# Performance work log

Measured on AMD Instinct MI355X. Metric: run time of the kernel, lower is better.

## Reference

```python
import jax, jax.numpy as jnp
import numpy as np

B, C, H, W = 4, 256, 64, 64
NHEAD = 8
KH = KW = 3          # partition = [3, 3] -> 9-token windows, stride 1, padding 1
EPS = 1e-5           # torch LayerNorm default


def setup_inputs() -> dict:
    key = jax.random.key(0)
    ks = jax.random.split(key, 3)
    s = 1.0 / np.sqrt(C)  # xavier-ish scale
    return {
        "src": jax.random.normal(ks[0], (B, C, H, W), jnp.float32),
        "ln_w": jnp.ones((C,), jnp.float32),
        "ln_b": jnp.zeros((C,), jnp.float32),
        "in_proj_w": jax.random.normal(ks[1], (3 * C, C), jnp.float32) * s,
        "in_proj_b": jnp.zeros((3 * C,), jnp.float32),
        "out_proj_w": jax.random.normal(ks[2], (C, C), jnp.float32) * s,
        "out_proj_b": jnp.zeros((C,), jnp.float32),
    }


def reference(src, ln_w, ln_b, in_proj_w, in_proj_b, out_proj_w, out_proj_b):
    b, c, h, w = src.shape
    L = h * w
    S = KH * KW  # 9 tokens per local window
    # --- Unfold: overlapping 3x3 windows, padding 1, stride 1 (torch.nn.Unfold order: c major, kernel pos minor)
    xp = jnp.pad(src, ((0, 0), (0, 0), (1, 1), (1, 1)))
    patches = jnp.stack(
        [xp[:, :, i : i + h, j : j + w] for i in range(KH) for j in range(KW)], axis=2
    )  # [b, c, 9, h, w]
    x = patches.reshape(b, c, S, L).transpose(2, 0, 3, 1).reshape(S, b * L, c)  # [S, bL, c]
    # --- Pre-norm (norm1); note: pos embed in the source is overwritten (q = k = src2), FFN is dead code
    mu = x.mean(-1, keepdims=True)
    var = ((x - mu) ** 2).mean(-1, keepdims=True)
    x2 = (x - mu) / jnp.sqrt(var + EPS) * ln_w + ln_b
    # --- MultiheadAttention (self-attn, eval mode -> no dropout)
    qkv = jnp.einsum("sbc,dc->sbd", x2, in_proj_w) + in_proj_b  # [S, bL, 3c]
    q, k, v = jnp.split(qkv, 3, axis=-1)
    dh = c // NHEAD
    scale = dh ** -0.5
    q = q.reshape(S, b * L, NHEAD, dh) * scale
    k = k.reshape(S, b * L, NHEAD, dh)
    v = v.reshape(S, b * L, NHEAD, dh)
    scores = jnp.einsum("sbhd,tbhd->bhst", q, k)        # [bL, H, 9, 9]
    attn = jax.nn.softmax(scores, axis=-1)
    o = jnp.einsum("bhst,tbhd->sbhd", attn, v).reshape(S, b * L, c)
    o = jnp.einsum("sbc,dc->sbd", o, out_proj_w) + out_proj_b
    y = x + o  # residual
    # --- Fold back (kernel 1x1, stride 1): each output pixel = its window's center token
    center = y[S // 2]  # [bL, c]
    return center.reshape(b, L, c).transpose(0, 2, 1).reshape(b, c, h, w)
```

## Files before the change

### kernel.cpp

```cpp
#include <hip/hip_runtime.h>
#include <math.h>


#define NPIX 16384
#define HW   4096
#define CDIM 256

typedef short  bf16x8 __attribute__((ext_vector_type(8)));
typedef float  f32x4  __attribute__((ext_vector_type(4)));
typedef unsigned short u16x8 __attribute__((ext_vector_type(8)));

__device__ inline float bf2f(unsigned short u) {
    unsigned v = ((unsigned)u) << 16;
    return __builtin_bit_cast(float, v);
}
__device__ inline unsigned short f2bf(float f) {
    unsigned u = __builtin_bit_cast(unsigned, f);
    u += 0x7FFFu + ((u >> 16) & 1u);
    return (unsigned short)(u >> 16);
}

__global__ __launch_bounds__(256) void k_prep(const float* __restrict__ Wqkv,
                                              const float* __restrict__ Wout,
                                              const float* __restrict__ bqkv,
                                              const float* __restrict__ lnb,
                                              unsigned short* __restrict__ Wqkvbf,
                                              unsigned short* __restrict__ Woutbf,
                                              float* __restrict__ pads) {
    int bid = blockIdx.x, t = threadIdx.x;
    if (bid < 768) {
        int i = bid * 256 + t;
        Wqkvbf[i] = f2bf(Wqkv[i]);
    } else if (bid < 1024) {
        int i = (bid - 768) * 256 + t;
        Woutbf[i] = f2bf(Wout[i]);
    } else {
        int d = (bid - 1024) * 256 + t;
        int row = 256 + d;
        const float* wrow = Wqkv + (size_t)row * CDIM;
        float s = bqkv[row];
        for (int c = 0; c < CDIM; ++c) s += lnb[c] * wrow[c];
        pads[d] = s;
    }
}

__device__ inline void stageW32(const unsigned short* __restrict__ g,
                                unsigned short* lds, int t) {
    int lane = t & 63;
    int wv   = t >> 6;
    int rin  = lane >> 2;
    int slot = lane & 3;
    #pragma unroll
    for (int it = 0; it < 4; ++it) {
        int rbase = (wv * 4 + it) * 16;
        int row = rbase + rin;
        const unsigned short* src = g + (size_t)row * 256 + ((slot ^ (row & 3)) * 8);
        __builtin_amdgcn_global_load_lds(
            (const __attribute__((address_space(1))) void*)src,
            (__attribute__((address_space(3))) void*)(lds + rbase * 32),
            16, 0, 0);
    }
}

__global__ __launch_bounds__(256) void k_ln_qkv(const float* __restrict__ src,
                                                const float* __restrict__ lnw,
                                                const float* __restrict__ lnb,
                                                const unsigned short* __restrict__ Wbf,
                                                const float* __restrict__ bias,
                                                unsigned short* __restrict__ qkvbf) {
    __shared__ unsigned short As[32 * 256];
    __shared__ unsigned short Bs[2][256 * 32];

    int t = threadIdx.x;
    int bid = blockIdx.x;
    int sb = (bid & 7) * 64 + (bid >> 3);
    int n0 = sb * 32;
    int b = n0 >> 12, p0 = n0 & 4095;

    stageW32(Wbf, Bs[0], t);

    float* red  = (float*)(&Bs[1][0]);
    float* red2 = red + 264;
    float* muv  = red + 528;
    float* rsv  = red + 560;
    int pix = t & 31, q = t >> 5;
    const float* sp = src + ((size_t)b * CDIM) * HW + p0 + pix;
    float x[32];
    float sum = 0.f, sq = 0.f;
    #pragma unroll
    for (int i = 0; i < 32; ++i) {
        x[i] = sp[(size_t)(q * 32 + i) * HW];
        sum += x[i]; sq += x[i] * x[i];
    }
    red[q * 33 + pix] = sum; red2[q * 33 + pix] = sq;
    __syncthreads();
    if (t < 32) {
        float s = 0.f, s2 = 0.f;
        #pragma unroll
        for (int qq = 0; qq < 8; ++qq) { s += red[qq * 33 + t]; s2 += red2[qq * 33 + t]; }
        float mu = s * (1.f / 256.f);
        float var = fmaxf(s2 * (1.f / 256.f) - mu * mu, 0.f);
        muv[t] = mu; rsv[t] = rsqrtf(var + 1e-5f);
    }
    __syncthreads();
    {
        float mu = muv[pix], rs = rsv[pix];
        #pragma unroll
        for (int c8 = 0; c8 < 4; ++c8) {
            u16x8 o8;
            #pragma unroll
            for (int j = 0; j < 8; ++j) {
                int c = q * 32 + c8 * 8 + j;
                float xn = (x[c8 * 8 + j] - mu) * rs * lnw[c] + lnb[c];
                o8[j] = f2bf(xn);
            }
            int chunk = q * 4 + c8;
            *(u16x8*)((char*)As + (pix * 512 + (((chunk & 7) ^ (pix & 7)) | (chunk & 24)) * 16)) = o8;
        }
    }
    __syncthreads();

    int lane = t & 63, wv = t >> 6;
    int lr = lane & 15, lg = lane >> 4;

    for (int pass = 0; pass < 3; ++pass) {
        f32x4 acc[2][4] = {};
        #pragma unroll
        for (int kc = 0; kc < 8; ++kc) {
            int s = pass * 8 + kc;
            if (s < 23) {
                int ns = s + 1;
                stageW32(Wbf + (size_t)((ns >> 3) * 256) * 256 + (ns & 7) * 32,
                         Bs[ns & 1], t);
            }
            const unsigned short* B = Bs[s & 1];
            int chA = kc * 4 + lg;
            bf16x8 a[2], bb[4];
            #pragma unroll
            for (int i = 0; i < 2; ++i) {
                int r = i * 16 + lr;
                int sl = ((chA & 7) ^ (r & 7)) | (chA & 24);
                a[i] = *(bf16x8*)((char*)As + (r * 512 + sl * 16));
            }
            #pragma unroll
            for (int j = 0; j < 4; ++j) {
                int rb = wv * 64 + j * 16 + lr;
                bb[j] = *(bf16x8*)((char*)B + (rb * 64 + ((lg ^ (rb & 3)) * 16)));
            }
            #pragma unroll
            for (int i = 0; i < 2; ++i)
                #pragma unroll
                for (int j = 0; j < 4; ++j)
                    acc[i][j] = __builtin_amdgcn_mfma_f32_16x16x32_bf16(
                        a[i], bb[j], acc[i][j], 0, 0, 0);
            __syncthreads();
        }
        int d0 = pass * 256;
        unsigned short* Ct = (unsigned short*)Bs[1];
        #pragma unroll
        for (int j = 0; j < 4; ++j) {
            float bj = bias[d0 + wv * 64 + j * 16 + lr];
            #pragma unroll
            for (int i = 0; i < 2; ++i)
                #pragma unroll
                for (int r2 = 0; r2 < 4; ++r2) {
                    int row = i * 16 + lg * 4 + r2;
                    int col = wv * 64 + j * 16 + lr;
                    int chunk = col >> 3;
                    int sl = ((chunk & 7) ^ (row & 7)) | (chunk & 24);
                    Ct[row * 256 + sl * 8 + (col & 7)] = f2bf(acc[i][j][r2] + bj);
                }
        }
        __syncthreads();
        int row = t >> 3, cb = t & 7;
        #pragma unroll
        for (int s2 = 0; s2 < 4; ++s2) {
            int chunk = cb + 8 * s2;
            int sl = ((chunk & 7) ^ (row & 7)) | (chunk & 24);
            bf16x8 v = *(bf16x8*)(Ct + row * 256 + sl * 8);
            *(bf16x8*)(qkvbf + (size_t)(n0 + row) * 768 + d0 + chunk * 8) = v;
        }
        __syncthreads();
    }
}

__global__ __launch_bounds__(256) void k_attn_proj(const unsigned short* __restrict__ qkvbf,
                                                   const float* __restrict__ pads,
                                                   const unsigned short* __restrict__ Wbf,
                                                   const float* __restrict__ bias,
                                                   const float* __restrict__ src,
                                                   float* __restrict__ out) {
    __shared__ unsigned short Bt[32 * 264];
    __shared__ unsigned short As2[2][256 * 32];
    int t  = threadIdx.x;
    int bid = blockIdx.x;
    int sb  = (bid & 7) * 64 + (bid >> 3);
    int n0 = sb * 32;
    int b  = n0 >> 12;
    int p0 = n0 & 4095;

    stageW32(Wbf, As2[0], t);

    {
        int pix = t >> 3, h = t & 7;
        int n = n0 + pix;
        int p = n & 4095, hh0 = p >> 6, ww0 = p & 63;
        const float scale = 0.1767766952966369f;

        float qv[32];
        const unsigned short* qp = qkvbf + (size_t)n * 768 + h * 32;
        #pragma unroll
        for (int c8 = 0; c8 < 4; ++c8) {
            bf16x8 v = *(const bf16x8*)(qp + c8 * 8);
            #pragma unroll
            for (int j = 0; j < 8; ++j) qv[c8 * 8 + j] = bf2f((unsigned short)v[j]) * scale;
        }
        float sc[9];
        #pragma unroll
        for (int t9 = 0; t9 < 9; ++t9) {
            int dy = t9 / 3 - 1, dx = t9 % 3 - 1;
            int hh = hh0 + dy, ww = ww0 + dx;
            bool ok = ((unsigned)hh < 64u) && ((unsigned)ww < 64u);
            float a = 0.f;
            if (ok) {
                const unsigned short* kp = qkvbf + (size_t)(n + dy * 64 + dx) * 768 + 256 + h * 32;
                #pragma unroll
                for (int c8 = 0; c8 < 4; ++c8) {
                    bf16x8 v = *(const bf16x8*)(kp + c8 * 8);
                    #pragma unroll
                    for (int j = 0; j < 8; ++j) a += qv[c8 * 8 + j] * bf2f((unsigned short)v[j]);
                }
            } else {
                const float* pk = pads + h * 32;
                #pragma unroll
                for (int j = 0; j < 32; ++j) a += qv[j] * pk[j];
            }
            sc[t9] = a;
        }
        float m = sc[0];
        #pragma unroll
        for (int t9 = 1; t9 < 9; ++t9) m = fmaxf(m, sc[t9]);
        float s = 0.f;
        #pragma unroll
        for (int t9 = 0; t9 < 9; ++t9) { sc[t9] = __expf(sc[t9] - m); s += sc[t9]; }
        float inv = 1.0f / s;

        float ov[32];
        #pragma unroll
        for (int j = 0; j < 32; ++j) ov[j] = 0.f;
        #pragma unroll
        for (int t9 = 0; t9 < 9; ++t9) {
            int dy = t9 / 3 - 1, dx = t9 % 3 - 1;
            int hh = hh0 + dy, ww = ww0 + dx;
            bool ok = ((unsigned)hh < 64u) && ((unsigned)ww < 64u);
            float w = sc[t9] * inv;
            if (ok) {
                const unsigned short* vp = qkvbf + (size_t)(n + dy * 64 + dx) * 768 + 512 + h * 32;
                #pragma unroll
                for (int c8 = 0; c8 < 4; ++c8) {
                    bf16x8 v = *(const bf16x8*)(vp + c8 * 8);
                    #pragma unroll
                    for (int j = 0; j < 8; ++j) ov[c8 * 8 + j] += w * bf2f((unsigned short)v[j]);
                }
            } else {
                const float* pv = pads + 256 + h * 32;
                #pragma unroll
                for (int j = 0; j < 32; ++j) ov[j] += w * pv[j];
            }
        }
        #pragma unroll
        for (int c8 = 0; c8 < 4; ++c8) {
            u16x8 o8;
            #pragma unroll
            for (int j = 0; j < 8; ++j) o8[j] = f2bf(ov[c8 * 8 + j]);
            *(u16x8*)(Bt + pix * 264 + h * 32 + c8 * 8) = o8;
        }
    }
    __syncthreads();

    int lane = t & 63, wv = t >> 6;
    int lr = lane & 15, lg = lane >> 4;
    f32x4 acc[4][2] = {};
    #pragma unroll
    for (int kc = 0; kc < 8; ++kc) {
        if (kc < 7) stageW32(Wbf + (kc + 1) * 32, As2[(kc + 1) & 1], t);
        const unsigned short* A = As2[kc & 1];
        bf16x8 a[4], bb[2];
        #pragma unroll
        for (int i = 0; i < 4; ++i) {
            int r = wv * 64 + i * 16 + lr;
            a[i] = *(bf16x8*)((char*)A + (r * 64 + ((lg ^ (r & 3)) * 16)));
        }
        #pragma unroll
        for (int j = 0; j < 2; ++j)
            bb[j] = *(bf16x8*)(Bt + (j * 16 + lr) * 264 + kc * 32 + lg * 8);
        #pragma unroll
        for (int i = 0; i < 4; ++i)
            #pragma unroll
            for (int j = 0; j < 2; ++j)
                acc[i][j] = __builtin_amdgcn_mfma_f32_16x16x32_bf16(
                    a[i], bb[j], acc[i][j], 0, 0, 0);
        __syncthreads();
    }
    #pragma unroll
    for (int i = 0; i < 4; ++i) {
        #pragma unroll
        for (int r2 = 0; r2 < 4; ++r2) {
            int dg = wv * 64 + i * 16 + lg * 4 + r2;
            float bd = bias[dg];
            #pragma unroll
            for (int j = 0; j < 2; ++j) {
                int ng = p0 + j * 16 + lr;
                size_t idx = ((size_t)(b * CDIM + dg)) * HW + ng;
                out[idx] = acc[i][j][r2] + bd + src[idx];
            }
        }
    }
}

extern "C" void kernel_launch(void* const* d_in, const int* in_sizes, int n_in,
                              void* d_out, int out_size, void* d_ws, size_t ws_size,
                              hipStream_t stream) {
    const float* src  = (const float*)d_in[0];
    const float* lnw  = (const float*)d_in[1];
    const float* lnb  = (const float*)d_in[2];
    const float* Wqkv = (const float*)d_in[3];
    const float* bqkv = (const float*)d_in[4];
    const float* Wout = (const float*)d_in[5];
    const float* bout = (const float*)d_in[6];
    float* out = (float*)d_out;

    unsigned short* qkvbf  = (unsigned short*)d_ws;
    unsigned short* Wqkvbf = qkvbf + (size_t)NPIX * 768;
    unsigned short* Woutbf = Wqkvbf + 768 * 256;
    float* pads = (float*)(Woutbf + 256 * 256);

    k_prep<<<1026, 256, 0, stream>>>(Wqkv, Wout, bqkv, lnb, Wqkvbf, Woutbf, pads);
    k_ln_qkv<<<512, 256, 0, stream>>>(src, lnw, lnb, Wqkvbf, bqkv, qkvbf);
    k_attn_proj<<<512, 256, 0, stream>>>(qkvbf, pads, Woutbf, bout, src, out);
}
```

Before: 58.55 us.

## Read GEMM weight fragments directly from global memory instead of LDS staging

Both GEMM kernels drop the double-buffered global_load_lds staging of the bf16 weight tiles and instead load MFMA B/A fragments straight from global memory (expected L2-resident), removing per-k-step barriers and LDS footprint. The C staging buffer becomes a padded array without swizzle, and launch bounds request 3-4 blocks per CU to raise occupancy. The trade-off is more global/L2 traffic per wave with less latency hiding from explicit prefetch, and possible register pressure under the tighter bounds.

```diff
diff --git a/kernel.cpp b/kernel.cpp
--- a/kernel.cpp
+++ b/kernel.cpp
@@ -44,32 +44,14 @@
     }
 }
 
-__device__ inline void stageW32(const unsigned short* __restrict__ g,
-                                unsigned short* lds, int t) {
-    int lane = t & 63;
-    int wv   = t >> 6;
-    int rin  = lane >> 2;
-    int slot = lane & 3;
-    #pragma unroll
-    for (int it = 0; it < 4; ++it) {
-        int rbase = (wv * 4 + it) * 16;
-        int row = rbase + rin;
-        const unsigned short* src = g + (size_t)row * 256 + ((slot ^ (row & 3)) * 8);
-        __builtin_amdgcn_global_load_lds(
-            (const __attribute__((address_space(1))) void*)src,
-            (__attribute__((address_space(3))) void*)(lds + rbase * 32),
-            16, 0, 0);
-    }
-}
-
-__global__ __launch_bounds__(256) void k_ln_qkv(const float* __restrict__ src,
-                                                const float* __restrict__ lnw,
-                                                const float* __restrict__ lnb,
-                                                const unsigned short* __restrict__ Wbf,
-                                                const float* __restrict__ bias,
-                                                unsigned short* __restrict__ qkvbf) {
+__global__ __launch_bounds__(256, 3) void k_ln_qkv(const float* __restrict__ src,
+                                                   const float* __restrict__ lnw,
+                                                   const float* __restrict__ lnb,
+                                                   const unsigned short* __restrict__ Wbf,
+                                                   const float* __restrict__ bias,
+                                                   unsigned short* __restrict__ qkvbf) {
     __shared__ unsigned short As[32 * 256];
-    __shared__ unsigned short Bs[2][256 * 32];
+    __shared__ unsigned short Ct[32 * 264];
 
     int t = threadIdx.x;
     int bid = blockIdx.x;
@@ -77,33 +59,31 @@
     int n0 = sb * 32;
     int b = n0 >> 12, p0 = n0 & 4095;
 
-    stageW32(Wbf, Bs[0], t);
-
-    float* red  = (float*)(&Bs[1][0]);
-    float* red2 = red + 264;
-    float* muv  = red + 528;
-    float* rsv  = red + 560;
-    int pix = t & 31, q = t >> 5;
-    const float* sp = src + ((size_t)b * CDIM) * HW + p0 + pix;
-    float x[32];
-    float sum = 0.f, sq = 0.f;
-    #pragma unroll
-    for (int i = 0; i < 32; ++i) {
-        x[i] = sp[(size_t)(q * 32 + i) * HW];
-        sum += x[i]; sq += x[i] * x[i];
-    }
-    red[q * 33 + pix] = sum; red2[q * 33 + pix] = sq;
-    __syncthreads();
-    if (t < 32) {
-        float s = 0.f, s2 = 0.f;
-        #pragma unroll
-        for (int qq = 0; qq < 8; ++qq) { s += red[qq * 33 + t]; s2 += red2[qq * 33 + t]; }
-        float mu = s * (1.f / 256.f);
-        float var = fmaxf(s2 * (1.f / 256.f) - mu * mu, 0.f);
-        muv[t] = mu; rsv[t] = rsqrtf(var + 1e-5f);
-    }
-    __syncthreads();
     {
+        float* red  = (float*)Ct;
+        float* red2 = red + 264;
+        float* muv  = red + 528;
+        float* rsv  = red + 560;
+        int pix = t & 31, q = t >> 5;
+        const float* sp = src + ((size_t)b * CDIM) * HW + p0 + pix;
+        float x[32];
+        float sum = 0.f, sq = 0.f;
+        #pragma unroll
+        for (int i = 0; i < 32; ++i) {
+            x[i] = sp[(size_t)(q * 32 + i) * HW];
+            sum += x[i]; sq += x[i] * x[i];
+        }
+        red[q * 33 + pix] = sum; red2[q * 33 + pix] = sq;
+        __syncthreads();
+        if (t < 32) {
+            float s = 0.f, s2 = 0.f;
+            #pragma unroll
+            for (int qq = 0; qq < 8; ++qq) { s += red[qq * 33 + t]; s2 += red2[qq * 33 + t]; }
+            float mu = s * (1.f / 256.f);
+            float var = fmaxf(s2 * (1.f / 256.f) - mu * mu, 0.f);
+            muv[t] = mu; rsv[t] = rsqrtf(var + 1e-5f);
+        }
+        __syncthreads();
         float mu = muv[pix], rs = rsv[pix];
         #pragma unroll
         for (int c8 = 0; c8 < 4; ++c8) {
@@ -124,82 +104,66 @@
     int lr = lane & 15, lg = lane >> 4;
 
     for (int pass = 0; pass < 3; ++pass) {
+        int d0 = pass * 256;
         f32x4 acc[2][4] = {};
-        #pragma unroll
-        for (int kc = 0; kc < 8; ++kc) {
-            int s = pass * 8 + kc;
-            if (s < 23) {
-                int ns = s + 1;
-                stageW32(Wbf + (size_t)((ns >> 3) * 256) * 256 + (ns & 7) * 32,
-                         Bs[ns & 1], t);
-            }
-            const unsigned short* B = Bs[s & 1];
-            int chA = kc * 4 + lg;
-            bf16x8 a[2], bb[4];
-            #pragma unroll
-            for (int i = 0; i < 2; ++i) {
-                int r = i * 16 + lr;
-                int sl = ((chA & 7) ^ (r & 7)) | (chA & 24);
-                a[i] = *(bf16x8*)((char*)As + (r * 512 + sl * 16));
-            }
-            #pragma unroll
-            for (int j = 0; j < 4; ++j) {
-                int rb = wv * 64 + j * 16 + lr;
-                bb[j] = *(bf16x8*)((char*)B + (rb * 64 + ((lg ^ (rb & 3)) * 16)));
-            }
-            #pragma unroll
-            for (int i = 0; i < 2; ++i)
+        for (int c = 0; c < 4; ++c) {
+            #pragma unroll
+            for (int kk = 0; kk < 2; ++kk) {
+                int chA = c * 8 + kk * 4 + lg;
+                bf16x8 a[2], bb[4];
+                #pragma unroll
+                for (int i = 0; i < 2; ++i) {
+                    int r = i * 16 + lr;
+                    int sl = ((chA & 7) ^ (r & 7)) | (chA & 24);
+                    a[i] = *(bf16x8*)((char*)As + (r * 512 + sl * 16));
+                }
                 #pragma unroll
                 for (int j = 0; j < 4; ++j)
-                    acc[i][j] = __builtin_amdgcn_mfma_f32_16x16x32_bf16(
-                        a[i], bb[j], acc[i][j], 0, 0, 0);
-            __syncthreads();
-        }
-        int d0 = pass * 256;
-        unsigned short* Ct = (unsigned short*)Bs[1];
+                    bb[j] = *(const bf16x8*)(Wbf +
+                        (size_t)(d0 + wv * 64 + j * 16 + lr) * 256 + c * 64 + kk * 32 + lg * 8);
+                #pragma unroll
+                for (int i = 0; i < 2; ++i)
+                    #pragma unroll
+                    for (int j = 0; j < 4; ++j)
+                        acc[i][j] = __builtin_amdgcn_mfma_f32_16x16x32_bf16(
+                            a[i], bb[j], acc[i][j], 0, 0, 0);
+            }
+        }
+        __syncthreads();
         #pragma unroll
         for (int j = 0; j < 4; ++j) {
             float bj = bias[d0 + wv * 64 + j * 16 + lr];
             #pragma unroll
             for (int i = 0; i < 2; ++i)
                 #pragma unroll
-                for (int r2 = 0; r2 < 4; ++r2) {
-                    int row = i * 16 + lg * 4 + r2;
-                    int col = wv * 64 + j * 16 + lr;
-                    int chunk = col >> 3;
-                    int sl = ((chunk & 7) ^ (row & 7)) | (chunk & 24);
-                    Ct[row * 256 + sl * 8 + (col & 7)] = f2bf(acc[i][j][r2] + bj);
-                }
+                for (int r2 = 0; r2 < 4; ++r2)
+                    Ct[(i * 16 + lg * 4 + r2) * 264 + wv * 64 + j * 16 + lr] =
+                        f2bf(acc[i][j][r2] + bj);
         }
         __syncthreads();
         int row = t >> 3, cb = t & 7;
         #pragma unroll
         for (int s2 = 0; s2 < 4; ++s2) {
             int chunk = cb + 8 * s2;
-            int sl = ((chunk & 7) ^ (row & 7)) | (chunk & 24);
-            bf16x8 v = *(bf16x8*)(Ct + row * 256 + sl * 8);
+            bf16x8 v = *(bf16x8*)(Ct + row * 264 + chunk * 8);
             *(bf16x8*)(qkvbf + (size_t)(n0 + row) * 768 + d0 + chunk * 8) = v;
         }
-        __syncthreads();
-    }
-}
-
-__global__ __launch_bounds__(256) void k_attn_proj(const unsigned short* __restrict__ qkvbf,
-                                                   const float* __restrict__ pads,
-                                                   const unsigned short* __restrict__ Wbf,
-                                                   const float* __restrict__ bias,
-                                                   const float* __restrict__ src,
-                                                   float* __restrict__ out) {
+    }
+}
+
+__global__ __launch_bounds__(256, 4) void k_attn_proj(const unsigned short* __restrict__ qkvbf,
+                                                      const float* __restrict__ pads,
+                                                      const unsigned short* __restrict__ Wbf,
+                                                      const float* __restrict__ bias,
+                                                      const float* __restrict__ src,
+                                                      float* __restrict__ out) {
     __shared__ unsigned short Bt[32 * 264];
-    __shared__ unsigned short As2[2][256 * 32];
     int t  = threadIdx.x;
     int bid = blockIdx.x;
     int sb  = (bid & 7) * 64 + (bid >> 3);
     int n0 = sb * 32;
     int b  = n0 >> 12;
     int p0 = n0 & 4095;
-
-    stageW32(Wbf, As2[0], t);
 
     {
         int pix = t >> 3, h = t & 7;
@@ -281,16 +245,12 @@
     int lane = t & 63, wv = t >> 6;
     int lr = lane & 15, lg = lane >> 4;
     f32x4 acc[4][2] = {};
-    #pragma unroll
     for (int kc = 0; kc < 8; ++kc) {
-        if (kc < 7) stageW32(Wbf + (kc + 1) * 32, As2[(kc + 1) & 1], t);
-        const unsigned short* A = As2[kc & 1];
         bf16x8 a[4], bb[2];
         #pragma unroll
-        for (int i = 0; i < 4; ++i) {
-            int r = wv * 64 + i * 16 + lr;
-            a[i] = *(bf16x8*)((char*)A + (r * 64 + ((lg ^ (r & 3)) * 16)));
-        }
+        for (int i = 0; i < 4; ++i)
+            a[i] = *(const bf16x8*)(Wbf +
+                (size_t)(wv * 64 + i * 16 + lr) * 256 + kc * 32 + lg * 8);
         #pragma unroll
         for (int j = 0; j < 2; ++j)
             bb[j] = *(bf16x8*)(Bt + (j * 16 + lr) * 264 + kc * 32 + lg * 8);
@@ -300,7 +260,6 @@
             for (int j = 0; j < 2; ++j)
                 acc[i][j] = __builtin_amdgcn_mfma_f32_16x16x32_bf16(
                     a[i], bb[j], acc[i][j], 0, 0, 0);
-        __syncthreads();
     }
     #pragma unroll
     for (int i = 0; i < 4; ++i) {
```

After: 70.53 us. 20.5% more time.
